# Performance work log

Hardware: AMD Instinct MI355X
Metric: run time of the kernel (lower is better)

## Reference

```python
import jax, jax.numpy as jnp
import numpy as np

N, C, T, V, S, IC = 128, 256, 32, 25, 3, 64  # batch, channels, frames, joints, subsets, inter_channels
EPS = 1e-5


def conv1x1(x, w, b):
    # x: [N,C,T,V], w: [O,C], b: [O]
    return jnp.einsum('nctv,oc->notv', x, w) + b[None, :, None, None]


def bn(x, g, be, m, v):
    # eval-mode BatchNorm2d over channel dim
    inv = g / jnp.sqrt(v + EPS)
    return x * inv[None, :, None, None] + (be - m * inv)[None, :, None, None]


def pe_spatial(c, v):
    # spatial positional encoding: position = joint id, same for every frame
    div = jnp.exp(jnp.arange(0, c, 2).astype(jnp.float32) * (-(np.log(10000.0) / c)))
    ang = jnp.arange(v, dtype=jnp.float32)[:, None] * div[None, :]  # [V, C/2]
    pe = jnp.stack([jnp.sin(ang), jnp.cos(ang)], axis=-1).reshape(v, c)  # interleave sin/cos -> [V,C]
    return pe.T[None, :, None, :]  # [1,C,1,V]


def setup_inputs() -> dict:
    key = jax.random.key(0)
    ks = jax.random.split(key, 40)
    rn = lambda i, sh, s=1.0: jax.random.normal(ks[i], sh, dtype=jnp.float32) * s
    ru = lambda i, sh: jax.random.uniform(ks[i], sh, dtype=jnp.float32, minval=0.5, maxval=1.5)
    d = {
        'x': rn(0, (N, C, T, V)),
        'in_w': rn(1, (2 * S * IC, C), 0.05), 'in_b': rn(2, (2 * S * IC,), 0.05),
        'alphas': jnp.ones((1, S, 1, 1), jnp.float32),
        'attention0s': jnp.ones((1, S, V, V), jnp.float32) / V,
        'out_w': rn(3, (C, S * C), 0.02), 'out_b': rn(4, (C,), 0.02),
    }
    i = 5
    for p, (ci, co) in [('d1', (C, C)), ('d2', (C, C)), ('ff', (C, C))]:
        d[p + '_w'] = rn(i, (co, ci), 0.05); i += 1
        d[p + '_b'] = rn(i, (co,), 0.05); i += 1
    for p in ['out', 'd1', 'd2', 'ff']:
        d[p + '_g'] = 1.0 + rn(i, (C,), 0.1); i += 1
        d[p + '_be'] = rn(i, (C,), 0.1); i += 1
        d[p + '_m'] = rn(i, (C,), 0.1); i += 1
        d[p + '_v'] = ru(i, (C,)); i += 1
    return d


def reference(x, in_w, in_b, alphas, attention0s, out_w, out_b,
              d1_w, d1_b, d2_w, d2_b, ff_w, ff_b,
              out_g, out_be, out_m, out_v,
              d1_g, d1_be, d1_m, d1_v,
              d2_g, d2_be, d2_m, d2_v,
              ff_g, ff_be, ff_m, ff_v):
    n, c, t, v = x.shape
    lrelu = lambda z: jnp.where(z >= 0, z, 0.1 * z)
    # spatial positional encoding
    y = x + pe_spatial(c, v)
    # QK projection via 1x1 conv, split into q,k: [N,S,IC,T,V]
    qk = conv1x1(y, in_w, in_b).reshape(n, 2 * S, IC, t, v)
    q, k = qk[:, :S], qk[:, S:]
    # tanh-based attention score + learnable global attention (atts buffer is zeros)
    att = jnp.tanh(jnp.einsum('nsctu,nsctv->nsuv', q, k) / (IC * t)) * alphas
    att = att + attention0s  # broadcast over batch (dropout p=0 -> identity)
    # aggregate: [N,S,C,T,V] -> [N, S*C, T, V]
    y = jnp.einsum('nctu,nsuv->nsctv', x, att).reshape(n, S * c, t, v)
    # out_nets: conv1x1 + BN
    y = bn(conv1x1(y, out_w, out_b), out_g, out_be, out_m, out_v)
    # residual 1
    y = lrelu(bn(conv1x1(x, d1_w, d1_b), d1_g, d1_be, d1_m, d1_v) + y)
    # ff_nets: conv1x1 + BN + LeakyReLU
    y = lrelu(bn(conv1x1(y, ff_w, ff_b), ff_g, ff_be, ff_m, ff_v))
    # residual 2
    y = lrelu(bn(conv1x1(x, d2_w, d2_b), d2_g, d2_be, d2_m, d2_v) + y)
    return y
```

## Files before the change

### kernel.cpp

```cpp
#include <hip/hip_runtime.h>

typedef unsigned short u16;
typedef __bf16 bf16x8 __attribute__((ext_vector_type(8)));
typedef float f32x4 __attribute__((ext_vector_type(4)));

constexpr int NB = 128;
constexpr int CC = 256;
constexpr int TT = 32;
constexpr int VV = 25;
constexpr int SSS = 3;
constexpr int PIX = 800;
constexpr float EPSV = 1e-5f;

constexpr size_t OFF_PE  = 0;
constexpr size_t OFF_W1  = 64*1024;
constexpr size_t OFF_WK2 = OFF_W1  + 256*1024;
constexpr size_t OFF_WFF = OFF_WK2 + 512*1024;
constexpr size_t OFF_WD2 = OFF_WFF + 128*1024;
constexpr size_t OFF_B1  = OFF_WD2 + 128*1024;
constexpr size_t OFF_BK2 = OFF_B1  + 4096;
constexpr size_t OFF_BFF = OFF_BK2 + 4096;
constexpr size_t OFF_BD2 = OFF_BFF + 4096;
constexpr size_t OFF_ATT = 2ull*1024*1024;
constexpr size_t OFF_XB  = 4ull*1024*1024;
constexpr size_t OFF_BIG = OFF_XB + 52428800ull;
constexpr size_t OFF_Y3  = OFF_BIG + 157286400ull;

__device__ __forceinline__ float bf2f(u16 h) {
  union { unsigned u; float f; } c; c.u = ((unsigned)h) << 16; return c.f;
}
__device__ __forceinline__ u16 f2bf(float f) {
  union { float f; unsigned u; } c; c.f = f;
  unsigned r = c.u + 0x7fffu + ((c.u >> 16) & 1u);
  return (u16)(r >> 16);
}
__device__ __forceinline__ float lrelu(float z) { return z >= 0.f ? z : 0.1f*z; }

__global__ void prep_k(
    const float* __restrict__ in_w,  const float* __restrict__ in_b,
    const float* __restrict__ out_w, const float* __restrict__ out_b,
    const float* __restrict__ d1_w,  const float* __restrict__ d1_b,
    const float* __restrict__ d2_w,  const float* __restrict__ d2_b,
    const float* __restrict__ ff_w,  const float* __restrict__ ff_b,
    const float* __restrict__ out_g, const float* __restrict__ out_be, const float* __restrict__ out_m, const float* __restrict__ out_v,
    const float* __restrict__ d1_g,  const float* __restrict__ d1_be,  const float* __restrict__ d1_m,  const float* __restrict__ d1_v,
    const float* __restrict__ d2_g,  const float* __restrict__ d2_be,  const float* __restrict__ d2_m,  const float* __restrict__ d2_v,
    const float* __restrict__ ff_g,  const float* __restrict__ ff_be,  const float* __restrict__ ff_m,  const float* __restrict__ ff_v,
    float* __restrict__ pe, u16* __restrict__ w1b, float* __restrict__ b1,
    u16* __restrict__ wk2, float* __restrict__ bk2,
    u16* __restrict__ wff, float* __restrict__ bff,
    u16* __restrict__ wd2, float* __restrict__ bd2,
    u16* __restrict__ qkb)
{
  const int id  = blockIdx.x*blockDim.x + threadIdx.x;
  const int nth = gridDim.x*blockDim.x;
  for (int i = id; i < CC*VV; i += nth) {
    int ch = i / VV, vv = i - ch*VV;
    int j = ch >> 1;
    float ang = (float)vv * expf((float)j * (-2.0f*logf(10000.0f)/(float)CC));
    pe[i] = (ch & 1) ? cosf(ang) : sinf(ang);
  }
  for (int i = id; i < 384*CC; i += nth) w1b[i] = f2bf(in_w[i]);
  for (int i = id; i < 384;    i += nth) b1[i] = in_b[i];
  for (int i = id; i < CC*1024; i += nth) {
    int o = i >> 10, k = i & 1023;
    float w;
    if (k < 768) { float inv = out_g[o]*rsqrtf(out_v[o]+EPSV); w = out_w[o*768+k]*inv; }
    else         { float inv = d1_g[o]*rsqrtf(d1_v[o]+EPSV);   w = d1_w[o*256+(k-768)]*inv; }
    wk2[i] = f2bf(w);
  }
  for (int i = id; i < CC*CC; i += nth) {
    int o = i >> 8;
    wff[i] = f2bf(ff_w[i]*(ff_g[o]*rsqrtf(ff_v[o]+EPSV)));
    wd2[i] = f2bf(d2_w[i]*(d2_g[o]*rsqrtf(d2_v[o]+EPSV)));
  }
  for (int i = id; i < CC; i += nth) {
    float invo = out_g[i]*rsqrtf(out_v[i]+EPSV);
    float invd = d1_g[i]*rsqrtf(d1_v[i]+EPSV);
    bk2[i] = out_b[i]*invo + out_be[i] - out_m[i]*invo
           + d1_b[i]*invd  + d1_be[i]  - d1_m[i]*invd;
    float invf = ff_g[i]*rsqrtf(ff_v[i]+EPSV);
    bff[i] = ff_b[i]*invf + ff_be[i] - ff_m[i]*invf;
    float inv2 = d2_g[i]*rsqrtf(d2_v[i]+EPSV);
    bd2[i] = d2_b[i]*inv2 + d2_be[i] - d2_m[i]*inv2;
  }
  for (int i = id; i < NB*TT*7*384; i += nth) {
    int ch = i % 384; int r = i / 384;
    int pr = r % 7; int t = (r/7) % TT; int n = r / (7*TT);
    qkb[((size_t)n*1024 + (size_t)t*32 + 25 + pr)*384 + ch] = 0;
  }
}

__global__ __launch_bounds__(256) void k0_pe_cvt(
    const float* __restrict__ x, const float* __restrict__ pe,
    u16* __restrict__ yb, u16* __restrict__ xb)
{
  __shared__ float xt[CC*VV];
  __shared__ float pl[CC*VV];
  const int t = blockIdx.x, n = blockIdx.y;
  const float* xs = x + (size_t)n*CC*PIX + t*VV;
  for (int f = threadIdx.x; f < CC*VV; f += 256) {
    int c = f / VV, u = f - c*VV;
    xt[f] = xs[(size_t)c*PIX + u];
    pl[f] = pe[f];
  }
  __syncthreads();
  const int c = threadIdx.x;
  u16* yrow = yb + ((size_t)n*PIX + t*VV)*CC + c;
  u16* xrow = xb + ((size_t)n*PIX + t*VV)*CC + c;
  #pragma unroll
  for (int u = 0; u < VV; ++u) {
    float xv = xt[c*VV+u];
    yrow[(size_t)u*CC] = f2bf(xv + pl[c*VV+u]);
    xrow[(size_t)u*CC] = f2bf(xv);
  }
}

__global__ __launch_bounds__(64) void att_k(
    const u16* __restrict__ qkb, const float* __restrict__ alphas,
    const float* __restrict__ att0, u16* __restrict__ attb)
{
  const int s = blockIdx.x, n = blockIdx.y, lane = threadIdx.x;
  const u16* qb = qkb + (size_t)n*1024*384 + s*64;
  const u16* kb = qb + 192;
  f32x4 acc[2][2];
  #pragma unroll
  for (int i = 0; i < 2; ++i)
    #pragma unroll
    for (int j = 0; j < 2; ++j) acc[i][j] = f32x4{0.f,0.f,0.f,0.f};

  for (int t = 0; t < TT; ++t) {
    const u16* qrow = qb + (size_t)t*32*384;
    const u16* krow = kb + (size_t)t*32*384;
    #pragma unroll
    for (int ks = 0; ks < 2; ++ks) {
      const int ko = ks*32 + (lane>>4)*8;
      bf16x8 a0 = *(const bf16x8*)(qrow + (size_t)(lane&15)*384 + ko);
      bf16x8 a1 = *(const bf16x8*)(qrow + (size_t)(16+(lane&15))*384 + ko);
      bf16x8 b0 = *(const bf16x8*)(krow + (size_t)(lane&15)*384 + ko);
      bf16x8 b1 = *(const bf16x8*)(krow + (size_t)(16+(lane&15))*384 + ko);
      acc[0][0] = __builtin_amdgcn_mfma_f32_16x16x32_bf16(a0, b0, acc[0][0], 0,0,0);
      acc[0][1] = __builtin_amdgcn_mfma_f32_16x16x32_bf16(a0, b1, acc[0][1], 0,0,0);
      acc[1][0] = __builtin_amdgcn_mfma_f32_16x16x32_bf16(a1, b0, acc[1][0], 0,0,0);
      acc[1][1] = __builtin_amdgcn_mfma_f32_16x16x32_bf16(a1, b1, acc[1][1], 0,0,0);
    }
  }
  const float alpha = alphas[s];
  const float sc = 1.0f/2048.0f;
  u16* ab = attb + ((size_t)n*SSS + s)*1024;
  #pragma unroll
  for (int fm = 0; fm < 2; ++fm)
    #pragma unroll
    for (int fn = 0; fn < 2; ++fn)
      #pragma unroll
      for (int j = 0; j < 4; ++j) {
        int u = fm*16 + (lane>>4)*4 + j;
        int v = fn*16 + (lane&15);
        float val = 0.f;
        if (u < VV && v < VV)
          val = tanhf(acc[fm][fn][j]*sc)*alpha + att0[s*VV*VV + u*VV + v];
        ab[v*32 + u] = f2bf(val);
      }
}

__global__ __launch_bounds__(256) void p_k2(
    const float* __restrict__ x, const u16* __restrict__ attb, u16* __restrict__ Pb)
{
  __shared__ u16 Xs[CC*40];
  __shared__ u16 Al[SSS*32*40];
  const int t = blockIdx.x, n = blockIdx.y;
  const float* xs = x + (size_t)n*CC*PIX + t*VV;
  for (int f = threadIdx.x; f < CC*VV; f += 256) {
    int c = f / VV, u = f - c*VV;
    Xs[c*40+u] = f2bf(xs[(size_t)c*PIX + u]);
  }
  for (int idx = threadIdx.x; idx < CC*7; idx += 256) {
    int c = idx / 7, u = 25 + idx % 7;
    Xs[c*40+u] = 0;
  }
  const u16* ab = attb + (size_t)n*SSS*1024;
  for (int f = threadIdx.x; f < SSS*1024; f += 256) {
    int sv = f >> 5, u = f & 31;
    Al[sv*40+u] = ab[f];
  }
  __syncthreads();

  const int lane = threadIdx.x & 63, w = threadIdx.x >> 6;
  const int cb0 = w*64;
  const int k0 = (lane>>4)*8;
  const int r15 = lane & 15;
  f32x4 acc[SSS][4][2];
  #pragma unroll
  for (int s = 0; s < SSS; ++s)
    #pragma unroll
    for (int mt = 0; mt < 4; ++mt)
      #pragma unroll
      for (int nt = 0; nt < 2; ++nt) acc[s][mt][nt] = f32x4{0.f,0.f,0.f,0.f};

  #pragma unroll
  for (int s = 0; s < SSS; ++s) {
    bf16x8 b0 = *(const bf16x8*)&Al[((s*32) + r15)*40 + k0];
    bf16x8 b1 = *(const bf16x8*)&Al[((s*32) + 16 + r15)*40 + k0];
    #pragma unroll
    for (int mt = 0; mt < 4; ++mt) {
      bf16x8 a = *(const bf16x8*)&Xs[(cb0 + mt*16 + r15)*40 + k0];
      acc[s][mt][0] = __builtin_amdgcn_mfma_f32_16x16x32_bf16(a, b0, acc[s][mt][0], 0,0,0);
      acc[s][mt][1] = __builtin_amdgcn_mfma_f32_16x16x32_bf16(a, b1, acc[s][mt][1], 0,0,0);
    }
  }

  const int j4 = (lane>>4)*4;
  #pragma unroll
  for (int s = 0; s < SSS; ++s)
    #pragma unroll
    for (int nt = 0; nt < 2; ++nt) {
      const int v = nt*16 + r15;
      if (v < VV) {
        u16* dst0 = Pb + ((size_t)n*PIX + t*VV + v)*768 + s*CC + cb0 + j4;
        #pragma unroll
        for (int mt = 0; mt < 4; ++mt) {
          f32x4 a = acc[s][mt][nt];
          ushort4 st; st.x=f2bf(a[0]); st.y=f2bf(a[1]); st.z=f2bf(a[2]); st.w=f2bf(a[3]);
          *(ushort4*)(dst0 + mt*16) = st;
        }
      }
    }
}

template<int KTOT, int NKC0, int BS0, int BS1, int EPI>
__global__ __launch_bounds__(512, 1)
void gemm_k(const u16* __restrict__ W, const float* __restrict__ bias,
            const u16* __restrict__ B0, const u16* __restrict__ B1,
            void* __restrict__ outv, const u16* __restrict__ y4b)
{
  constexpr int NKC = KTOT/64;
  __shared__ u16 As[2][128*64];
  __shared__ u16 Bs[2][160*64];
  const int tid = threadIdx.x;
  const int lane = tid & 63, wid = tid >> 6;
  const int wm = wid >> 1, wn = wid & 1;
  const int pt = blockIdx.x, mt = blockIdx.y, n = blockIdx.z;
  const int m0 = mt*128, p0 = pt*160;
  const int lr = lane >> 3;
  const int lc = (((lane & 7) ^ lr)) * 8;

  f32x4 acc[2][5];
  #pragma unroll
  for (int i = 0; i < 2; ++i)
    #pragma unroll
    for (int j = 0; j < 5; ++j) acc[i][j] = f32x4{0.f,0.f,0.f,0.f};

  auto stage = [&](int buf, int kc) {
    const u16* wsrc = W + (size_t)m0*KTOT + (size_t)kc*64;
    for (int g = wid; g < 16; g += 8) {
      const u16* src = wsrc + (size_t)(g*8 + lr)*KTOT + lc;
      __builtin_amdgcn_global_load_lds(
          (const __attribute__((address_space(1))) void*)src,
          (__attribute__((address_space(3))) void*)(&As[buf][g*512]), 16, 0, 0);
    }
    const u16* bbase; int bs;
    if (NKC0 >= NKC || kc < NKC0) {
      bbase = B0 + ((size_t)n*PIX + p0)*BS0 + (size_t)kc*64; bs = BS0;
    } else {
      bbase = B1 + ((size_t)n*PIX + p0)*BS1 + (size_t)(kc-NKC0)*64; bs = BS1;
    }
    for (int g = wid; g < 20; g += 8) {
      const u16* src = bbase + (size_t)(g*8 + lr)*bs + lc;
      __builtin_amdgcn_global_load_lds(
          (const __attribute__((address_space(1))) void*)src,
          (__attribute__((address_space(3))) void*)(&Bs[buf][g*512]), 16, 0, 0);
    }
  };

  auto compute = [&](int buf) {
    const int par = lane & 7;
    const int gq  = lane >> 4;
    const int r15 = lane & 15;
    #pragma unroll
    for (int ks = 0; ks < 2; ++ks) {
      const int ko = (((ks*4 + gq) ^ par)) * 8;
      bf16x8 a0 = *(const bf16x8*)&As[buf][(wm*32 + r15)*64 + ko];
      bf16x8 a1 = *(const bf16x8*)&As[buf][(wm*32 + 16 + r15)*64 + ko];
      bf16x8 bfr[5];
      #pragma unroll
      for (int fn = 0; fn < 5; ++fn)
        bfr[fn] = *(const bf16x8*)&Bs[buf][(wn*80 + fn*16 + r15)*64 + ko];
      #pragma unroll
      for (int fn = 0; fn < 5; ++fn) {
        acc[0][fn] = __builtin_amdgcn_mfma_f32_16x16x32_bf16(a0, bfr[fn], acc[0][fn], 0,0,0);
        acc[1][fn] = __builtin_amdgcn_mfma_f32_16x16x32_bf16(a1, bfr[fn], acc[1][fn], 0,0,0);
      }
    }
  };

  stage(0, 0);
  __syncthreads();
  for (int kc = 0; kc < NKC; ++kc) {
    if (kc + 1 < NKC) stage((kc+1)&1, kc+1);
    compute(kc&1);
    __syncthreads();
  }

  const int oc = (lane>>4)*4, pc = lane&15;
  #pragma unroll
  for (int fm = 0; fm < 2; ++fm) {
    const int o = m0 + wm*32 + fm*16 + oc;
    const float4 bv = *(const float4*)&bias[o];
    #pragma unroll
    for (int fn = 0; fn < 5; ++fn) {
      const int p = p0 + wn*80 + fn*16 + pc;
      f32x4 v = acc[fm][fn];
      float r0 = v[0]+bv.x, r1 = v[1]+bv.y, r2 = v[2]+bv.z, r3 = v[3]+bv.w;
      if constexpr (EPI == 0) {
        int row = (p/VV)*32 + (p%VV);
        ushort4 st; st.x=f2bf(r0); st.y=f2bf(r1); st.z=f2bf(r2); st.w=f2bf(r3);
        *(ushort4*)((u16*)outv + ((size_t)n*1024 + row)*384 + o) = st;
      } else if constexpr (EPI == 1) {
        ushort4 st;
        st.x=f2bf(lrelu(r0)); st.y=f2bf(lrelu(r1)); st.z=f2bf(lrelu(r2)); st.w=f2bf(lrelu(r3));
        *(ushort4*)((u16*)outv + ((size_t)n*PIX + p)*256 + o) = st;
      } else if constexpr (EPI == 2) {
        u16* op = (u16*)outv + ((size_t)n*256 + o)*PIX + p;
        op[0]      = f2bf(lrelu(r0));
        op[PIX]    = f2bf(lrelu(r1));
        op[2*PIX]  = f2bf(lrelu(r2));
        op[3*PIX]  = f2bf(lrelu(r3));
      } else {
        const u16* yp = y4b + ((size_t)n*256 + o)*PIX + p;
        float* op = (float*)outv + ((size_t)n*256 + o)*PIX + p;
        op[0]      = lrelu(r0 + bf2f(yp[0]));
        op[PIX]    = lrelu(r1 + bf2f(yp[PIX]));
        op[2*PIX]  = lrelu(r2 + bf2f(yp[2*PIX]));
        op[3*PIX]  = lrelu(r3 + bf2f(yp[3*PIX]));
      }
    }
  }
}

extern "C" void kernel_launch(void* const* d_in, const int* in_sizes, int n_in,
                              void* d_out, int out_size, void* d_ws, size_t ws_size,
                              hipStream_t stream)
{
  const float* x      = (const float*)d_in[0];
  const float* in_w   = (const float*)d_in[1];
  const float* in_b   = (const float*)d_in[2];
  const float* alphas = (const float*)d_in[3];
  const float* att0   = (const float*)d_in[4];
  const float* out_w  = (const float*)d_in[5];
  const float* out_b  = (const float*)d_in[6];
  const float* d1_w   = (const float*)d_in[7];
  const float* d1_b   = (const float*)d_in[8];
  const float* d2_w   = (const float*)d_in[9];
  const float* d2_b   = (const float*)d_in[10];
  const float* ff_w   = (const float*)d_in[11];
  const float* ff_b   = (const float*)d_in[12];
  const float* out_g  = (const float*)d_in[13];
  const float* out_be = (const float*)d_in[14];
  const float* out_m  = (const float*)d_in[15];
  const float* out_v  = (const float*)d_in[16];
  const float* d1_g   = (const float*)d_in[17];
  const float* d1_be  = (const float*)d_in[18];
  const float* d1_m   = (const float*)d_in[19];
  const float* d1_v   = (const float*)d_in[20];
  const float* d2_g   = (const float*)d_in[21];
  const float* d2_be  = (const float*)d_in[22];
  const float* d2_m   = (const float*)d_in[23];
  const float* d2_v   = (const float*)d_in[24];
  const float* ff_g   = (const float*)d_in[25];
  const float* ff_be  = (const float*)d_in[26];
  const float* ff_m   = (const float*)d_in[27];
  const float* ff_v   = (const float*)d_in[28];

  char* ws = (char*)d_ws;
  float* pe  = (float*)(ws + OFF_PE);
  u16*  w1b  = (u16*)(ws + OFF_W1);
  u16*  wk2  = (u16*)(ws + OFF_WK2);
  u16*  wff  = (u16*)(ws + OFF_WFF);
  u16*  wd2  = (u16*)(ws + OFF_WD2);
  float* b1  = (float*)(ws + OFF_B1);
  float* bk2 = (float*)(ws + OFF_BK2);
  float* bff = (float*)(ws + OFF_BFF);
  float* bd2 = (float*)(ws + OFF_BD2);
  u16*  attb = (u16*)(ws + OFF_ATT);
  u16*  xb   = (u16*)(ws + OFF_XB);
  u16*  qkb  = (u16*)(ws + OFF_BIG);
  u16*  Pb   = (u16*)(ws + OFF_BIG);
  u16*  y4b  = (u16*)(ws + OFF_BIG);
  u16*  yb   = (u16*)(ws + OFF_Y3);
  u16*  y3b  = (u16*)(ws + OFF_Y3);

  prep_k<<<256, 256, 0, stream>>>(
      in_w, in_b, out_w, out_b, d1_w, d1_b, d2_w, d2_b, ff_w, ff_b,
      out_g, out_be, out_m, out_v, d1_g, d1_be, d1_m, d1_v,
      d2_g, d2_be, d2_m, d2_v, ff_g, ff_be, ff_m, ff_v,
      pe, w1b, b1, wk2, bk2, wff, bff, wd2, bd2, qkb);

  k0_pe_cvt<<<dim3(TT, NB), 256, 0, stream>>>(x, pe, yb, xb);

  gemm_k<256, 4, 256, 256, 0><<<dim3(5, 3, NB), 512, 0, stream>>>(w1b, b1, yb, yb, qkb, nullptr);

  att_k<<<dim3(SSS, NB), 64, 0, stream>>>(qkb, alphas, att0, attb);

  p_k2<<<dim3(TT, NB), 256, 0, stream>>>(x, attb, Pb);

  gemm_k<1024, 12, 768, 256, 1><<<dim3(5, 2, NB), 512, 0, stream>>>(wk2, bk2, Pb, xb, y3b, nullptr);

  gemm_k<256, 4, 256, 256, 2><<<dim3(5, 2, NB), 512, 0, stream>>>(wff, bff, y3b, y3b, y4b, nullptr);

  gemm_k<256, 4, 256, 256, 3><<<dim3(5, 2, NB), 512, 0, stream>>>(wd2, bd2, xb, xb, d_out, y4b);
}
```

Baseline: 640.0 us.

## Fold positional encoding into per-joint QK bias and reuse bf16 x in aggregation

Because the positional encoding depends only on channel and joint, W·(x+pe)+b is rewritten as W·x plus a per-joint bias W·pe+b, computed once by a small new kernel. The conversion kernel then no longer writes a separate bf16 (x+pe) tensor, and the QK GEMM reads the shared bf16 x buffer. The aggregation kernel also loads bf16 x instead of re-reading and converting fp32 x. This removes a full activation write and some fp32 reads, in exchange for an extra tiny launch and a per-pixel bias gather in the GEMM epilogue. Rounding changes slightly because pe is no longer added before bf16 conversion.

```diff
diff --git a/kernel.cpp b/kernel.cpp
--- a/kernel.cpp
+++ b/kernel.cpp
@@ -18,7 +18,7 @@
 constexpr size_t OFF_WFF = OFF_WK2 + 512*1024;
 constexpr size_t OFF_WD2 = OFF_WFF + 128*1024;
 constexpr size_t OFF_B1  = OFF_WD2 + 128*1024;
-constexpr size_t OFF_BK2 = OFF_B1  + 4096;
+constexpr size_t OFF_BK2 = OFF_B1  + 48*1024;
 constexpr size_t OFF_BFF = OFF_BK2 + 4096;
 constexpr size_t OFF_BD2 = OFF_BFF + 4096;
 constexpr size_t OFF_ATT = 2ull*1024*1024;
@@ -46,7 +46,7 @@
     const float* __restrict__ d1_g,  const float* __restrict__ d1_be,  const float* __restrict__ d1_m,  const float* __restrict__ d1_v,
     const float* __restrict__ d2_g,  const float* __restrict__ d2_be,  const float* __restrict__ d2_m,  const float* __restrict__ d2_v,
     const float* __restrict__ ff_g,  const float* __restrict__ ff_be,  const float* __restrict__ ff_m,  const float* __restrict__ ff_v,
-    float* __restrict__ pe, u16* __restrict__ w1b, float* __restrict__ b1,
+    float* __restrict__ pe, u16* __restrict__ w1b,
     u16* __restrict__ wk2, float* __restrict__ bk2,
     u16* __restrict__ wff, float* __restrict__ bff,
     u16* __restrict__ wd2, float* __restrict__ bd2,
@@ -61,7 +61,6 @@
     pe[i] = (ch & 1) ? cosf(ang) : sinf(ang);
   }
   for (int i = id; i < 384*CC; i += nth) w1b[i] = f2bf(in_w[i]);
-  for (int i = id; i < 384;    i += nth) b1[i] = in_b[i];
   for (int i = id; i < CC*1024; i += nth) {
     int o = i >> 10, k = i & 1023;
     float w;
@@ -91,29 +90,34 @@
   }
 }
 
-__global__ __launch_bounds__(256) void k0_pe_cvt(
-    const float* __restrict__ x, const float* __restrict__ pe,
-    u16* __restrict__ yb, u16* __restrict__ xb)
+__global__ __launch_bounds__(256) void prep2_k(
+    const float* __restrict__ in_w, const float* __restrict__ in_b,
+    const float* __restrict__ pe, float* __restrict__ b1v)
+{
+  const int i = blockIdx.x*blockDim.x + threadIdx.x;
+  if (i >= 384*VV) return;
+  const int o = i % 384, v = i / 384;
+  float acc = in_b[o];
+  for (int c = 0; c < CC; ++c) acc += in_w[o*CC+c]*pe[c*VV+v];
+  b1v[v*384+o] = acc;
+}
+
+__global__ __launch_bounds__(256) void k0_cvt(
+    const float* __restrict__ x, u16* __restrict__ xb)
 {
   __shared__ float xt[CC*VV];
-  __shared__ float pl[CC*VV];
   const int t = blockIdx.x, n = blockIdx.y;
   const float* xs = x + (size_t)n*CC*PIX + t*VV;
   for (int f = threadIdx.x; f < CC*VV; f += 256) {
     int c = f / VV, u = f - c*VV;
     xt[f] = xs[(size_t)c*PIX + u];
-    pl[f] = pe[f];
   }
   __syncthreads();
   const int c = threadIdx.x;
-  u16* yrow = yb + ((size_t)n*PIX + t*VV)*CC + c;
   u16* xrow = xb + ((size_t)n*PIX + t*VV)*CC + c;
   #pragma unroll
-  for (int u = 0; u < VV; ++u) {
-    float xv = xt[c*VV+u];
-    yrow[(size_t)u*CC] = f2bf(xv + pl[c*VV+u]);
-    xrow[(size_t)u*CC] = f2bf(xv);
-  }
+  for (int u = 0; u < VV; ++u)
+    xrow[(size_t)u*CC] = f2bf(xt[c*VV+u]);
 }
 
 __global__ __launch_bounds__(64) void att_k(
@@ -164,15 +168,15 @@
 }
 
 __global__ __launch_bounds__(256) void p_k2(
-    const float* __restrict__ x, const u16* __restrict__ attb, u16* __restrict__ Pb)
+    const u16* __restrict__ xb, const u16* __restrict__ attb, u16* __restrict__ Pb)
 {
   __shared__ u16 Xs[CC*40];
   __shared__ u16 Al[SSS*32*40];
   const int t = blockIdx.x, n = blockIdx.y;
-  const float* xs = x + (size_t)n*CC*PIX + t*VV;
-  for (int f = threadIdx.x; f < CC*VV; f += 256) {
-    int c = f / VV, u = f - c*VV;
-    Xs[c*40+u] = f2bf(xs[(size_t)c*PIX + u]);
+  const u16* xrow = xb + ((size_t)n*PIX + t*VV)*CC;
+  for (int f = threadIdx.x; f < VV*CC; f += 256) {
+    int u = f >> 8, c = f & 255;
+    Xs[c*40+u] = xrow[(size_t)u*CC + c];
   }
   for (int idx = threadIdx.x; idx < CC*7; idx += 256) {
     int c = idx / 7, u = 25 + idx % 7;
@@ -305,11 +309,13 @@
   #pragma unroll
   for (int fm = 0; fm < 2; ++fm) {
     const int o = m0 + wm*32 + fm*16 + oc;
-    const float4 bv = *(const float4*)&bias[o];
     #pragma unroll
     for (int fn = 0; fn < 5; ++fn) {
       const int p = p0 + wn*80 + fn*16 + pc;
       f32x4 v = acc[fm][fn];
+      float4 bv;
+      if constexpr (EPI == 0) bv = *(const float4*)&bias[(p % VV)*384 + o];
+      else                    bv = *(const float4*)&bias[o];
       float r0 = v[0]+bv.x, r1 = v[1]+bv.y, r2 = v[2]+bv.z, r3 = v[3]+bv.w;
       if constexpr (EPI == 0) {
         int row = (p/VV)*32 + (p%VV);
@@ -377,7 +383,7 @@
   u16*  wk2  = (u16*)(ws + OFF_WK2);
   u16*  wff  = (u16*)(ws + OFF_WFF);
   u16*  wd2  = (u16*)(ws + OFF_WD2);
-  float* b1  = (float*)(ws + OFF_B1);
+  float* b1v = (float*)(ws + OFF_B1);
   float* bk2 = (float*)(ws + OFF_BK2);
   float* bff = (float*)(ws + OFF_BFF);
   float* bd2 = (float*)(ws + OFF_BD2);
@@ -386,22 +392,23 @@
   u16*  qkb  = (u16*)(ws + OFF_BIG);
   u16*  Pb   = (u16*)(ws + OFF_BIG);
   u16*  y4b  = (u16*)(ws + OFF_BIG);
-  u16*  yb   = (u16*)(ws + OFF_Y3);
   u16*  y3b  = (u16*)(ws + OFF_Y3);
 
   prep_k<<<256, 256, 0, stream>>>(
       in_w, in_b, out_w, out_b, d1_w, d1_b, d2_w, d2_b, ff_w, ff_b,
       out_g, out_be, out_m, out_v, d1_g, d1_be, d1_m, d1_v,
       d2_g, d2_be, d2_m, d2_v, ff_g, ff_be, ff_m, ff_v,
-      pe, w1b, b1, wk2, bk2, wff, bff, wd2, bd2, qkb);
-
-  k0_pe_cvt<<<dim3(TT, NB), 256, 0, stream>>>(x, pe, yb, xb);
-
-  gemm_k<256, 4, 256, 256, 0><<<dim3(5, 3, NB), 512, 0, stream>>>(w1b, b1, yb, yb, qkb, nullptr);
+      pe, w1b, wk2, bk2, wff, bff, wd2, bd2, qkb);
+
+  prep2_k<<<(384*VV + 255)/256, 256, 0, stream>>>(in_w, in_b, pe, b1v);
+
+  k0_cvt<<<dim3(TT, NB), 256, 0, stream>>>(x, xb);
+
+  gemm_k<256, 4, 256, 256, 0><<<dim3(5, 3, NB), 512, 0, stream>>>(w1b, b1v, xb, xb, qkb, nullptr);
 
   att_k<<<dim3(SSS, NB), 64, 0, stream>>>(qkb, alphas, att0, attb);
 
-  p_k2<<<dim3(TT, NB), 256, 0, stream>>>(x, attb, Pb);
+  p_k2<<<dim3(TT, NB), 256, 0, stream>>>(xb, attb, Pb);
 
   gemm_k<1024, 12, 768, 256, 1><<<dim3(5, 2, NB), 512, 0, stream>>>(wk2, bk2, Pb, xb, y3b, nullptr);
 
```

Result: faster. 613.6 us (-4.1%).
